# Kernel optimization log

Hardware: AMD Instinct MI355X
Metric: run time of the kernel (lower is better)

## Reference

```python
import jax, jax.numpy as jnp
import numpy as np

B, L, H, T_MAX, D_ID, D_SZ, D_POS = 64, 1024, 256, 128, 128, 64, 128
V_ID, V_SZ = 65536, 256


def setup_inputs() -> dict:
    key = jax.random.key(0)
    ks = jax.random.split(key, 16)
    s = 0.02
    inp = {
        'obj_id': jax.random.randint(ks[0], (B,), 0, V_ID, dtype=jnp.int32),
        'obj_size': jax.random.randint(ks[1], (B,), 0, V_SZ, dtype=jnp.int32),
        'cache_lines': jax.random.randint(ks[2], (B, L), 0, V_ID, dtype=jnp.int32),
        'lengths': jax.random.randint(ks[3], (B,), 0, L, dtype=jnp.int32),
        'c0': jax.random.normal(ks[4], (B, H), jnp.float32),
        'h0': jax.random.normal(ks[5], (B, H), jnp.float32),
        'history': jax.random.normal(ks[6], (B, T_MAX - 1, H), jnp.float32),
        # learned parameters
        'obj_id_table': jax.random.normal(ks[7], (V_ID, D_ID), jnp.float32) * s,
        'obj_size_table': jax.random.normal(ks[8], (V_SZ, D_SZ), jnp.float32) * s,
        'pos_table': jax.random.normal(ks[9], (T_MAX, D_POS), jnp.float32) * s,
        'W_ih': jax.random.normal(ks[10], (4 * H, D_ID + D_SZ), jnp.float32) * s,
        'W_hh': jax.random.normal(ks[11], (4 * H, H), jnp.float32) * s,
        'b_ih': jnp.zeros((4 * H,), jnp.float32),
        'b_hh': jnp.zeros((4 * H,), jnp.float32),
        'attn_W': jax.random.normal(ks[12], (D_ID, H), jnp.float32) * s,
        'scorer_W': jax.random.normal(ks[13], (1, H + D_POS), jnp.float32) * s,
        'scorer_b': jnp.zeros((1,), jnp.float32),
        'reuse_W': jax.random.normal(ks[14], (1, H + D_POS), jnp.float32) * s,
        'reuse_b': jnp.zeros((1,), jnp.float32),
    }
    return inp


def reference(obj_id, obj_size, cache_lines, lengths, c0, h0, history,
              obj_id_table, obj_size_table, pos_table,
              W_ih, W_hh, b_ih, b_hh, attn_W,
              scorer_W, scorer_b, reuse_W, reuse_b):
    # --- embed current access and run one LSTMCell step ---
    x = jnp.concatenate([obj_id_table[obj_id], obj_size_table[obj_size]], axis=-1)  # (B, D_ID+D_SZ)
    gates = x @ W_ih.T + b_ih + h0 @ W_hh.T + b_hh  # (B, 4H)
    i, f, g, o = jnp.split(gates, 4, axis=-1)
    c = jax.nn.sigmoid(f) * c0 + jax.nn.sigmoid(i) * jnp.tanh(g)
    h = jax.nn.sigmoid(o) * jnp.tanh(c)

    # --- growing hidden-state history (deque bounded at max_attention_history) ---
    hist = jnp.concatenate([history, h[:, None, :]], axis=1)  # (B, T, H)
    T = hist.shape[1]
    pos = jnp.broadcast_to(pos_table[:T][None], (hist.shape[0], T, pos_table.shape[1]))
    values = jnp.concatenate([hist, pos], axis=-1)  # (B, T, H+P)

    # --- cache line embeddings (cache_lines_embedder == obj_id_embedder) ---
    q = obj_id_table[cache_lines]  # (B, L, D_ID)

    # --- General (bilinear) multi-query attention over history ---
    scores = jnp.einsum('bld,dh,bth->blt', q, attn_W, hist)  # (B, L, T)
    weights = jax.nn.softmax(scores, axis=-1)
    contexts = jnp.einsum('blt,btv->blv', weights, values)  # (B, L, H+P)

    # --- heads ---
    line_scores = jax.nn.softmax((contexts @ scorer_W.T + scorer_b)[..., 0], axis=-1)  # (B, L)
    pred_reuse = (contexts @ reuse_W.T + reuse_b)[..., 0]  # (B, L)

    # --- mask_renormalize over valid (unpadded) cache lines ---
    valid = jnp.maximum(lengths, 1)[:, None]  # min_len=1 in pad()
    mask = (jnp.arange(line_scores.shape[1])[None, :] < valid).astype(line_scores.dtype)
    masked = line_scores * mask
    denom = masked.sum(axis=-1, keepdims=True)
    probs = masked / jnp.where(denom > 0, denom, 1.0)
    return probs, pred_reuse
```

## Files before the change

kernel.cpp:

```cpp
#include <hip/hip_runtime.h>
#include <math.h>

#define BB 64
#define LL 1024
#define HH 256
#define TT 128
#define D_ID 128
#define D_SZ 64
#define D_POS 128
#define DX 192

typedef short s16x8 __attribute__((ext_vector_type(8)));
typedef float f32x16 __attribute__((ext_vector_type(16)));
typedef unsigned short u16x8 __attribute__((ext_vector_type(8)));
typedef unsigned short u16x4 __attribute__((ext_vector_type(4)));

__device__ __forceinline__ unsigned short f2bf(float f) {
    unsigned u = __float_as_uint(f);
    unsigned r = u + 0x7fffu + ((u >> 16) & 1u);
    return (unsigned short)(r >> 16);
}

__device__ __forceinline__ s16x8 pack8(float4 a, float4 b) {
    u16x8 p;
    p[0] = f2bf(a.x); p[1] = f2bf(a.y); p[2] = f2bf(a.z); p[3] = f2bf(a.w);
    p[4] = f2bf(b.x); p[5] = f2bf(b.y); p[6] = f2bf(b.z); p[7] = f2bf(b.w);
    return (s16x8)p;
}

__global__ void gates_kernel(const int* __restrict__ obj_id,
                             const int* __restrict__ obj_size,
                             const float* __restrict__ h0,
                             const float* __restrict__ c0,
                             const float* __restrict__ obj_id_table,
                             const float* __restrict__ obj_size_table,
                             const float* __restrict__ history,
                             const float* __restrict__ pos_table,
                             const float* __restrict__ W_ih,
                             const float* __restrict__ W_hh,
                             const float* __restrict__ b_ih,
                             const float* __restrict__ b_hh,
                             const float* __restrict__ scorer_W,
                             const float* __restrict__ reuse_W,
                             float* __restrict__ h_new,
                             float* __restrict__ sv,
                             float* __restrict__ rv) {
    int tid = threadIdx.x;

    if (blockIdx.x >= HH) {
        int b = blockIdx.x - HH;
        int which = tid >> 7;
        int t = tid & 127;
        if (t == TT - 1) return;
        const float* w = which ? reuse_W : scorer_W;
        const float* hrow = history + ((size_t)b * (TT - 1) + t) * HH;
        float acc = 0.f;
#pragma unroll 8
        for (int k = 0; k < HH / 4; ++k) {
            float4 hv = *(const float4*)(hrow + 4 * k);
            float4 wv = *(const float4*)(w + 4 * k);
            acc += hv.x * wv.x + hv.y * wv.y + hv.z * wv.z + hv.w * wv.w;
        }
        const float* prow = pos_table + (size_t)t * D_POS;
#pragma unroll 8
        for (int k = 0; k < D_POS / 4; ++k) {
            float4 pv = *(const float4*)(prow + 4 * k);
            float4 wv = *(const float4*)(w + HH + 4 * k);
            acc += pv.x * wv.x + pv.y * wv.y + pv.z * wv.z + pv.w * wv.w;
        }
        (which ? rv : sv)[b * TT + t] = acc;
        return;
    }

    __shared__ float xhS[224 * 64];
    __shared__ float gS[256];

    int j = blockIdx.x;
    int b = tid & 63;
    int q = __builtin_amdgcn_readfirstlane(tid >> 6);
    int r = q * HH + j;
    const float* wi = W_ih + (size_t)r * DX;
    const float* wh = W_hh + (size_t)r * HH;
    float acc = b_ih[r] + b_hh[r];

    int sb = tid >> 2;
    int c4 = tid & 3;

    {
        const float* row = obj_id_table + (size_t)obj_id[sb] * D_ID;
#pragma unroll
        for (int i = 0; i < 8; ++i) {
            int k = c4 * 4 + i * 16;
            float4 v = *(const float4*)(row + k);
            xhS[(k + 0) * 64 + sb] = v.x;
            xhS[(k + 1) * 64 + sb] = v.y;
            xhS[(k + 2) * 64 + sb] = v.z;
            xhS[(k + 3) * 64 + sb] = v.w;
        }
        const float* srow = obj_size_table + (size_t)obj_size[sb] * D_SZ;
#pragma unroll
        for (int i = 0; i < 4; ++i) {
            int k = c4 * 4 + i * 16;
            float4 v = *(const float4*)(srow + k);
            xhS[(D_ID + k + 0) * 64 + sb] = v.x;
            xhS[(D_ID + k + 1) * 64 + sb] = v.y;
            xhS[(D_ID + k + 2) * 64 + sb] = v.z;
            xhS[(D_ID + k + 3) * 64 + sb] = v.w;
        }
        const float* h0row = h0 + (size_t)sb * HH;
#pragma unroll
        for (int i = 0; i < 2; ++i) {
            int k = c4 * 4 + i * 16;
            float4 v = *(const float4*)(h0row + k);
            xhS[(DX + k + 0) * 64 + sb] = v.x;
            xhS[(DX + k + 1) * 64 + sb] = v.y;
            xhS[(DX + k + 2) * 64 + sb] = v.z;
            xhS[(DX + k + 3) * 64 + sb] = v.w;
        }
    }
    __syncthreads();
#pragma unroll 16
    for (int k = 0; k < DX; ++k)
        acc += wi[k] * xhS[k * 64 + b];
#pragma unroll 8
    for (int k = 0; k < 32; ++k)
        acc += wh[k] * xhS[(DX + k) * 64 + b];
    __syncthreads();

    {
        const float* h0row = h0 + (size_t)sb * HH + 32;
#pragma unroll
        for (int i = 0; i < 14; ++i) {
            int k = c4 * 4 + i * 16;
            float4 v = *(const float4*)(h0row + k);
            xhS[(k + 0) * 64 + sb] = v.x;
            xhS[(k + 1) * 64 + sb] = v.y;
            xhS[(k + 2) * 64 + sb] = v.z;
            xhS[(k + 3) * 64 + sb] = v.w;
        }
    }
    __syncthreads();
#pragma unroll 16
    for (int k = 0; k < 224; ++k)
        acc += wh[32 + k] * xhS[k * 64 + b];

    gS[q * 64 + b] = acc;
    __syncthreads();

    if (tid < 64) {
        float ig = 1.f / (1.f + expf(-gS[tid]));
        float fg = 1.f / (1.f + expf(-gS[64 + tid]));
        float gg = tanhf(gS[128 + tid]);
        float og = 1.f / (1.f + expf(-gS[192 + tid]));
        float c = fg * c0[tid * HH + j] + ig * gg;
        h_new[tid * HH + j] = og * tanhf(c);
    }
}

__global__ void attn_kernel(const int* __restrict__ cache_lines,
                            const float* __restrict__ obj_id_table,
                            const float* __restrict__ history,
                            const float* __restrict__ h_new,
                            const float* __restrict__ attn_W,
                            const float* __restrict__ pos_table,
                            const float* __restrict__ sv,
                            const float* __restrict__ rv,
                            const float* __restrict__ scorer_W,
                            const float* __restrict__ reuse_W,
                            const float* __restrict__ scorer_b,
                            const float* __restrict__ reuse_b,
                            float* __restrict__ logits,
                            float* __restrict__ out_reuse) {
    int b  = blockIdx.x >> 3;
    int l0 = (blockIdx.x & 7) * 128;
    int tid = threadIdx.x;
    __shared__ unsigned short qS[16384];
    __shared__ unsigned short hpS[16384];
    __shared__ float s127[2];

    int w = tid >> 6;
    int lane = tid & 63;
    int ln = lane & 31, half = lane >> 5;

    {
        int l = tid & 127;
        int cl = cache_lines[b * LL + l0 + l];
        const float* qrow = obj_id_table + (size_t)cl * D_ID;
        int lhi = (l >> 5) * 8, llo = l & 31;
#pragma unroll
        for (int i = 0; i < 8; ++i) {
            int u = 2 * i + (tid >> 7);
            float4 f0 = *(const float4*)(qrow + u * 8);
            float4 f1 = *(const float4*)(qrow + u * 8 + 4);
            *(s16x8*)(qS + (((lhi + (u >> 1)) * 64) + (u & 1) * 32 + llo) * 8) =
                pack8(f0, f1);
        }
    }

    {
        const float* arow = attn_W + (size_t)(32 * w + ln) * HH;
        const float* brow[4];
#pragma unroll
        for (int tt = 0; tt < 4; ++tt) {
            int t = tt * 32 + ln;
            brow[tt] = (t < TT - 1) ? history + ((size_t)b * (TT - 1) + t) * HH
                                    : h_new + (size_t)b * HH;
        }
        f32x16 pacc[4];
#pragma unroll
        for (int tt = 0; tt < 4; ++tt)
#pragma unroll
            for (int rr = 0; rr < 16; ++rr) pacc[tt][rr] = 0.f;

#pragma unroll 4
        for (int ks = 0; ks < 16; ++ks) {
            int off = ks * 16 + half * 8;
            float4 a0 = *(const float4*)(arow + off);
            float4 a1 = *(const float4*)(arow + off + 4);
            s16x8 af = pack8(a0, a1);
#pragma unroll
            for (int tt = 0; tt < 4; ++tt) {
                float4 b0 = *(const float4*)(brow[tt] + off);
                float4 b1 = *(const float4*)(brow[tt] + off + 4);
                pacc[tt] = __builtin_amdgcn_mfma_f32_32x32x16_bf16(
                    af, pack8(b0, b1), pacc[tt], 0, 0, 0);
            }
        }
#pragma unroll
        for (int tt = 0; tt < 4; ++tt)
#pragma unroll
            for (int qd = 0; qd < 4; ++qd) {
                u16x4 v;
                v[0] = f2bf(pacc[tt][4 * qd + 0]);
                v[1] = f2bf(pacc[tt][4 * qd + 1]);
                v[2] = f2bf(pacc[tt][4 * qd + 2]);
                v[3] = f2bf(pacc[tt][4 * qd + 3]);
                int sa = ((2 * w + (qd >> 1)) * 4 + tt) * 512 +
                         (qd & 1) * 256 + ln * 8 + 4 * half;
                *(u16x4*)(hpS + sa) = v;
            }
    }

    if (w < 2) {
        const float* wv = w ? reuse_W : scorer_W;
        float a = 0.f;
#pragma unroll
        for (int i = 0; i < 6; ++i) {
            int idx = lane + 64 * i;
            float x = (idx < HH)
                ? h_new[(size_t)b * HH + idx]
                : pos_table[(size_t)(TT - 1) * D_POS + (idx - HH)];
            a += wv[idx] * x;
        }
#pragma unroll
        for (int off = 1; off < 64; off <<= 1) a += __shfl_xor(a, off);
        if (lane == 0) s127[w] = a;
    }
    __syncthreads();

    f32x16 acc[4];
#pragma unroll
    for (int tt = 0; tt < 4; ++tt)
#pragma unroll
        for (int rr = 0; rr < 16; ++rr) acc[tt][rr] = 0.f;

    const unsigned short* qw = qS + w * 8 * 512;
#pragma unroll
    for (int k = 0; k < 8; ++k) {
        s16x8 a = *(const s16x8*)(qw + k * 512 + lane * 8);
#pragma unroll
        for (int tt = 0; tt < 4; ++tt) {
            s16x8 bf = *(const s16x8*)(hpS + (k * 4 + tt) * 512 + lane * 8);
            acc[tt] = __builtin_amdgcn_mfma_f32_32x32x16_bf16(a, bf, acc[tt], 0, 0, 0);
        }
    }

    float sv_r[4], rv_r[4];
#pragma unroll
    for (int tt = 0; tt < 4; ++tt) {
        sv_r[tt] = sv[b * TT + tt * 32 + ln];
        rv_r[tt] = rv[b * TT + tt * 32 + ln];
    }
    if (ln == 31) { sv_r[3] = s127[0]; rv_r[3] = s127[1]; }
    float sb = scorer_b[0], rb = reuse_b[0];

#pragma unroll
    for (int r = 0; r < 16; ++r) {
        float v0 = acc[0][r], v1 = acc[1][r], v2 = acc[2][r], v3 = acc[3][r];
        float m = fmaxf(fmaxf(v0, v1), fmaxf(v2, v3));
#pragma unroll
        for (int off = 1; off < 32; off <<= 1) m = fmaxf(m, __shfl_xor(m, off));
        float e0 = __expf(v0 - m), e1 = __expf(v1 - m),
              e2 = __expf(v2 - m), e3 = __expf(v3 - m);
        float s  = e0 + e1 + e2 + e3;
        float lg = e0 * sv_r[0] + e1 * sv_r[1] + e2 * sv_r[2] + e3 * sv_r[3];
        float rg = e0 * rv_r[0] + e1 * rv_r[1] + e2 * rv_r[2] + e3 * rv_r[3];
#pragma unroll
        for (int off = 1; off < 32; off <<= 1) {
            s  += __shfl_xor(s, off);
            lg += __shfl_xor(lg, off);
            rg += __shfl_xor(rg, off);
        }
        if (ln == 0) {
            int row = (r & 3) + 8 * (r >> 2) + 4 * half;
            int l = l0 + w * 32 + row;
            logits[b * LL + l] = lg / s + sb;
            out_reuse[b * LL + l] = rg / s + rb;
        }
    }
}

__global__ void finalsm_kernel(const float* __restrict__ logits,
                               const int* __restrict__ lengths,
                               float* __restrict__ out_probs) {
    int b = blockIdx.x;
    int tid = threadIdx.x;
    int valid = max(lengths[b], 1);
    float v[4];
    float m = -1e30f;
#pragma unroll
    for (int i = 0; i < 4; ++i) {
        int l = tid + 256 * i;
        v[i] = (l < valid) ? logits[b * LL + l] : -1e30f;
        m = fmaxf(m, v[i]);
    }
#pragma unroll
    for (int off = 1; off < 64; off <<= 1) m = fmaxf(m, __shfl_xor(m, off));
    __shared__ float redm[4];
    __shared__ float reds[4];
    int wave = tid >> 6;
    if ((tid & 63) == 0) redm[wave] = m;
    __syncthreads();
    m = fmaxf(fmaxf(redm[0], redm[1]), fmaxf(redm[2], redm[3]));
    float e[4];
    float s = 0.f;
#pragma unroll
    for (int i = 0; i < 4; ++i) {
        int l = tid + 256 * i;
        e[i] = (l < valid) ? expf(v[i] - m) : 0.f;
        s += e[i];
    }
#pragma unroll
    for (int off = 1; off < 64; off <<= 1) s += __shfl_xor(s, off);
    if ((tid & 63) == 0) reds[wave] = s;
    __syncthreads();
    s = reds[0] + reds[1] + reds[2] + reds[3];
    float inv = 1.f / s;
#pragma unroll
    for (int i = 0; i < 4; ++i)
        out_probs[b * LL + tid + 256 * i] = e[i] * inv;
}

extern "C" void kernel_launch(void* const* d_in, const int* in_sizes, int n_in,
                              void* d_out, int out_size, void* d_ws, size_t ws_size,
                              hipStream_t stream) {
    const int*   obj_id         = (const int*)d_in[0];
    const int*   obj_size       = (const int*)d_in[1];
    const int*   cache_lines    = (const int*)d_in[2];
    const int*   lengths        = (const int*)d_in[3];
    const float* c0             = (const float*)d_in[4];
    const float* h0             = (const float*)d_in[5];
    const float* history        = (const float*)d_in[6];
    const float* obj_id_table   = (const float*)d_in[7];
    const float* obj_size_table = (const float*)d_in[8];
    const float* pos_table      = (const float*)d_in[9];
    const float* W_ih           = (const float*)d_in[10];
    const float* W_hh           = (const float*)d_in[11];
    const float* b_ih           = (const float*)d_in[12];
    const float* b_hh           = (const float*)d_in[13];
    const float* attn_W         = (const float*)d_in[14];
    const float* scorer_W       = (const float*)d_in[15];
    const float* scorer_b       = (const float*)d_in[16];
    const float* reuse_W        = (const float*)d_in[17];
    const float* reuse_b        = (const float*)d_in[18];

    float* out = (float*)d_out;
    float* out_probs = out;
    float* out_reuse = out + BB * LL;

    char* ws = (char*)d_ws;
    float* h_new  = (float*)(ws);
    float* sv     = (float*)(ws + 65536);
    float* rv     = (float*)(ws + 98304);
    float* logits = (float*)(ws + 131072);

    hipLaunchKernelGGL(gates_kernel, dim3(HH + BB), dim3(256), 0, stream,
                       obj_id, obj_size, h0, c0, obj_id_table, obj_size_table,
                       history, pos_table, W_ih, W_hh, b_ih, b_hh,
                       scorer_W, reuse_W, h_new, sv, rv);
    hipLaunchKernelGGL(attn_kernel, dim3(BB * 8), dim3(256), 0, stream,
                       cache_lines, obj_id_table, history, h_new, attn_W,
                       pos_table, sv, rv, scorer_W, reuse_W,
                       scorer_b, reuse_b, logits, out_reuse);
    hipLaunchKernelGGL(finalsm_kernel, dim3(BB), dim3(256), 0, stream,
                       logits, lengths, out_probs);
}
```

Baseline: 193.0 us.

## Pre-convert obj_id table to bf16 and split LSTM input staging into prep kernel

Adds a prep kernel that converts the entire obj_id embedding table to bf16 in workspace, builds a transposed x/h0 buffer, and computes the history scorer/reuse dot products. The attention kernel then gathers bf16 query rows directly into MFMA A-fragment registers, dropping the LDS staging and fp32-to-bf16 packing. The gates kernel reads the prepared transposed buffer from global memory instead of staging it in LDS. This halves the bytes of the random query gather but adds a full-table read and write on every call plus an extra launch.

```diff
diff --git a/kernel.cpp b/kernel.cpp
--- a/kernel.cpp
+++ b/kernel.cpp
@@ -28,27 +28,35 @@
     return (s16x8)p;
 }
 
-__global__ void gates_kernel(const int* __restrict__ obj_id,
-                             const int* __restrict__ obj_size,
-                             const float* __restrict__ h0,
-                             const float* __restrict__ c0,
-                             const float* __restrict__ obj_id_table,
-                             const float* __restrict__ obj_size_table,
-                             const float* __restrict__ history,
-                             const float* __restrict__ pos_table,
-                             const float* __restrict__ W_ih,
-                             const float* __restrict__ W_hh,
-                             const float* __restrict__ b_ih,
-                             const float* __restrict__ b_hh,
-                             const float* __restrict__ scorer_W,
-                             const float* __restrict__ reuse_W,
-                             float* __restrict__ h_new,
-                             float* __restrict__ sv,
-                             float* __restrict__ rv) {
+__global__ void prep_kernel(const int* __restrict__ obj_id,
+                            const int* __restrict__ obj_size,
+                            const float* __restrict__ h0,
+                            const float* __restrict__ obj_id_table,
+                            const float* __restrict__ obj_size_table,
+                            const float* __restrict__ history,
+                            const float* __restrict__ pos_table,
+                            const float* __restrict__ scorer_W,
+                            const float* __restrict__ reuse_W,
+                            float* __restrict__ xh_t,
+                            float* __restrict__ sv,
+                            float* __restrict__ rv,
+                            unsigned short* __restrict__ qT) {
+    int blk = blockIdx.x;
     int tid = threadIdx.x;
 
-    if (blockIdx.x >= HH) {
-        int b = blockIdx.x - HH;
+    if (blk < 112) {
+        int b = tid & 63;
+        int k = blk * 4 + (tid >> 6);
+        float v;
+        if (k < D_ID)      v = obj_id_table[(size_t)obj_id[b] * D_ID + k];
+        else if (k < DX)   v = obj_size_table[(size_t)obj_size[b] * D_SZ + (k - D_ID)];
+        else               v = h0[b * HH + (k - DX)];
+        xh_t[k * 64 + b] = v;
+        return;
+    }
+
+    if (blk < 176) {
+        int b = blk - 112;
         int which = tid >> 7;
         int t = tid & 127;
         if (t == TT - 1) return;
@@ -72,78 +80,42 @@
         return;
     }
 
-    __shared__ float xhS[224 * 64];
-    __shared__ float gS[256];
-
+    {
+        size_t t0 = ((size_t)(blk - 176) * 256 + tid) * 32;
+        const float* src = obj_id_table + t0;
+        unsigned short* dst = qT + t0;
+#pragma unroll
+        for (int i = 0; i < 4; ++i) {
+            float4 a = *(const float4*)(src + i * 8);
+            float4 b = *(const float4*)(src + i * 8 + 4);
+            *(s16x8*)(dst + i * 8) = pack8(a, b);
+        }
+    }
+}
+
+__global__ void gates_kernel(const float* __restrict__ xh_t,
+                             const float* __restrict__ W_ih,
+                             const float* __restrict__ W_hh,
+                             const float* __restrict__ b_ih,
+                             const float* __restrict__ b_hh,
+                             const float* __restrict__ c0,
+                             float* __restrict__ h_new) {
     int j = blockIdx.x;
+    int tid = threadIdx.x;
     int b = tid & 63;
     int q = __builtin_amdgcn_readfirstlane(tid >> 6);
     int r = q * HH + j;
+    __shared__ float gS[256];
+
+    float acc = b_ih[r] + b_hh[r];
     const float* wi = W_ih + (size_t)r * DX;
     const float* wh = W_hh + (size_t)r * HH;
-    float acc = b_ih[r] + b_hh[r];
-
-    int sb = tid >> 2;
-    int c4 = tid & 3;
-
-    {
-        const float* row = obj_id_table + (size_t)obj_id[sb] * D_ID;
-#pragma unroll
-        for (int i = 0; i < 8; ++i) {
-            int k = c4 * 4 + i * 16;
-            float4 v = *(const float4*)(row + k);
-            xhS[(k + 0) * 64 + sb] = v.x;
-            xhS[(k + 1) * 64 + sb] = v.y;
-            xhS[(k + 2) * 64 + sb] = v.z;
-            xhS[(k + 3) * 64 + sb] = v.w;
-        }
-        const float* srow = obj_size_table + (size_t)obj_size[sb] * D_SZ;
-#pragma unroll
-        for (int i = 0; i < 4; ++i) {
-            int k = c4 * 4 + i * 16;
-            float4 v = *(const float4*)(srow + k);
-            xhS[(D_ID + k + 0) * 64 + sb] = v.x;
-            xhS[(D_ID + k + 1) * 64 + sb] = v.y;
-            xhS[(D_ID + k + 2) * 64 + sb] = v.z;
-            xhS[(D_ID + k + 3) * 64 + sb] = v.w;
-        }
-        const float* h0row = h0 + (size_t)sb * HH;
-#pragma unroll
-        for (int i = 0; i < 2; ++i) {
-            int k = c4 * 4 + i * 16;
-            float4 v = *(const float4*)(h0row + k);
-            xhS[(DX + k + 0) * 64 + sb] = v.x;
-            xhS[(DX + k + 1) * 64 + sb] = v.y;
-            xhS[(DX + k + 2) * 64 + sb] = v.z;
-            xhS[(DX + k + 3) * 64 + sb] = v.w;
-        }
-    }
-    __syncthreads();
 #pragma unroll 16
     for (int k = 0; k < DX; ++k)
-        acc += wi[k] * xhS[k * 64 + b];
-#pragma unroll 8
-    for (int k = 0; k < 32; ++k)
-        acc += wh[k] * xhS[(DX + k) * 64 + b];
-    __syncthreads();
-
-    {
-        const float* h0row = h0 + (size_t)sb * HH + 32;
-#pragma unroll
-        for (int i = 0; i < 14; ++i) {
-            int k = c4 * 4 + i * 16;
-            float4 v = *(const float4*)(h0row + k);
-            xhS[(k + 0) * 64 + sb] = v.x;
-            xhS[(k + 1) * 64 + sb] = v.y;
-            xhS[(k + 2) * 64 + sb] = v.z;
-            xhS[(k + 3) * 64 + sb] = v.w;
-        }
-    }
-    __syncthreads();
+        acc += wi[k] * xh_t[k * 64 + b];
 #pragma unroll 16
-    for (int k = 0; k < 224; ++k)
-        acc += wh[32 + k] * xhS[k * 64 + b];
-
+    for (int k = 0; k < HH; ++k)
+        acc += wh[k] * xh_t[(DX + k) * 64 + b];
     gS[q * 64 + b] = acc;
     __syncthreads();
 
@@ -158,7 +130,7 @@
 }
 
 __global__ void attn_kernel(const int* __restrict__ cache_lines,
-                            const float* __restrict__ obj_id_table,
+                            const unsigned short* __restrict__ qT,
                             const float* __restrict__ history,
                             const float* __restrict__ h_new,
                             const float* __restrict__ attn_W,
@@ -174,7 +146,6 @@
     int b  = blockIdx.x >> 3;
     int l0 = (blockIdx.x & 7) * 128;
     int tid = threadIdx.x;
-    __shared__ unsigned short qS[16384];
     __shared__ unsigned short hpS[16384];
     __shared__ float s127[2];
 
@@ -182,20 +153,12 @@
     int lane = tid & 63;
     int ln = lane & 31, half = lane >> 5;
 
-    {
-        int l = tid & 127;
-        int cl = cache_lines[b * LL + l0 + l];
-        const float* qrow = obj_id_table + (size_t)cl * D_ID;
-        int lhi = (l >> 5) * 8, llo = l & 31;
-#pragma unroll
-        for (int i = 0; i < 8; ++i) {
-            int u = 2 * i + (tid >> 7);
-            float4 f0 = *(const float4*)(qrow + u * 8);
-            float4 f1 = *(const float4*)(qrow + u * 8 + 4);
-            *(s16x8*)(qS + (((lhi + (u >> 1)) * 64) + (u & 1) * 32 + llo) * 8) =
-                pack8(f0, f1);
-        }
-    }
+    int cl = cache_lines[b * LL + l0 + w * 32 + ln];
+    const unsigned short* qrow = qT + (size_t)cl * D_ID + half * 8;
+    s16x8 qf[8];
+#pragma unroll
+    for (int ks = 0; ks < 8; ++ks)
+        qf[ks] = *(const s16x8*)(qrow + ks * 16);
 
     {
         const float* arow = attn_W + (size_t)(32 * w + ln) * HH;
@@ -264,14 +227,12 @@
 #pragma unroll
         for (int rr = 0; rr < 16; ++rr) acc[tt][rr] = 0.f;
 
-    const unsigned short* qw = qS + w * 8 * 512;
 #pragma unroll
     for (int k = 0; k < 8; ++k) {
-        s16x8 a = *(const s16x8*)(qw + k * 512 + lane * 8);
 #pragma unroll
         for (int tt = 0; tt < 4; ++tt) {
             s16x8 bf = *(const s16x8*)(hpS + (k * 4 + tt) * 512 + lane * 8);
-            acc[tt] = __builtin_amdgcn_mfma_f32_32x32x16_bf16(a, bf, acc[tt], 0, 0, 0);
+            acc[tt] = __builtin_amdgcn_mfma_f32_32x32x16_bf16(qf[k], bf, acc[tt], 0, 0, 0);
         }
     }
 
@@ -379,17 +340,21 @@
     float* out_reuse = out + BB * LL;
 
     char* ws = (char*)d_ws;
-    float* h_new  = (float*)(ws);
-    float* sv     = (float*)(ws + 65536);
-    float* rv     = (float*)(ws + 98304);
-    float* logits = (float*)(ws + 131072);
-
-    hipLaunchKernelGGL(gates_kernel, dim3(HH + BB), dim3(256), 0, stream,
-                       obj_id, obj_size, h0, c0, obj_id_table, obj_size_table,
-                       history, pos_table, W_ih, W_hh, b_ih, b_hh,
-                       scorer_W, reuse_W, h_new, sv, rv);
+    float*          h_new  = (float*)(ws);
+    float*          sv     = (float*)(ws + 65536);
+    float*          rv     = (float*)(ws + 98304);
+    float*          logits = (float*)(ws + 131072);
+    float*          xh_t   = (float*)(ws + 393216);
+    unsigned short* qT     = (unsigned short*)(ws + 1048576);
+
+    hipLaunchKernelGGL(prep_kernel, dim3(112 + 64 + 1024), dim3(256), 0, stream,
+                       obj_id, obj_size, h0, obj_id_table, obj_size_table,
+                       history, pos_table, scorer_W, reuse_W,
+                       xh_t, sv, rv, qT);
+    hipLaunchKernelGGL(gates_kernel, dim3(HH), dim3(256), 0, stream,
+                       xh_t, W_ih, W_hh, b_ih, b_hh, c0, h_new);
     hipLaunchKernelGGL(attn_kernel, dim3(BB * 8), dim3(256), 0, stream,
-                       cache_lines, obj_id_table, history, h_new, attn_W,
+                       cache_lines, qT, history, h_new, attn_W,
                        pos_table, sv, rv, scorer_W, reuse_W,
                        scorer_b, reuse_b, logits, out_reuse);
     hipLaunchKernelGGL(finalsm_kernel, dim3(BB), dim3(256), 0, stream,
```

After: 208.2 us. 1.08x slower.
